# Performance work log

Hardware: AMD Instinct MI355X
Metric: run time of the kernel (lower is better)

## Reference

```python
import jax, jax.numpy as jnp
import numpy as np

B, S, D = 2, 2048, 2048
HQ, HKV, HD, HDV = 32, 8, 64, 64
QPK = HQ // HKV
EPS = 1e-5


def setup_inputs() -> dict:
    key = jax.random.key(0)
    ks = jax.random.split(key, 10)
    s = lambda fan_in: 1.0 / np.sqrt(fan_in)
    return {
        'x': jax.random.normal(ks[0], (B, S, D), dtype=jnp.float32),
        'ln_g': jnp.ones((D,), jnp.float32),
        'ln_b': jnp.zeros((D,), jnp.float32),
        'Wq': jax.random.uniform(ks[1], (D, HQ * HD), jnp.float32, -s(D), s(D)),
        'bq': jax.random.uniform(ks[2], (HQ * HD,), jnp.float32, -s(D), s(D)),
        'Wk': jax.random.uniform(ks[3], (D, HKV * HD), jnp.float32, -s(D), s(D)),
        'bk': jax.random.uniform(ks[4], (HKV * HD,), jnp.float32, -s(D), s(D)),
        'Wv': jax.random.uniform(ks[5], (D, HKV * HDV), jnp.float32, -s(D), s(D)),
        'bv': jax.random.uniform(ks[6], (HKV * HDV,), jnp.float32, -s(D), s(D)),
        'Wo': jax.random.uniform(ks[7], (HQ * HDV, D), jnp.float32, -s(HQ * HDV), s(HQ * HDV)),
        'bo': jax.random.uniform(ks[8], (D,), jnp.float32, -s(HQ * HDV), s(HQ * HDV)),
    }


def reference(x, ln_g, ln_b, Wq, bq, Wk, bk, Wv, bv, Wo, bo):
    # LayerNorm
    mu = jnp.mean(x, axis=-1, keepdims=True)
    var = jnp.mean(jnp.square(x - mu), axis=-1, keepdims=True)
    xn = (x - mu) * jax.lax.rsqrt(var + EPS) * ln_g + ln_b

    q = (xn @ Wq + bq).reshape(B, S, HKV, QPK, HD) * (1.0 / np.sqrt(HD))
    k = (xn @ Wk + bk).reshape(B, S, HKV, HD)
    v = (xn @ Wv + bv).reshape(B, S, HKV, HDV)

    # scores: (b, t=query, T=key, h, q_per_kv)
    scores = jnp.einsum('bthqd,bThd->btThq', q, k)
    # causal mask: -inf where T > t (upper triangle above diagonal)
    mask = jnp.triu(jnp.full((S, S), -jnp.inf, dtype=scores.dtype), 1)
    scores = scores + mask[None, :, :, None, None]
    # NOTE: source softmaxes over dim=-4, i.e. the QUERY axis t -> axis=1 here
    scores = jax.nn.softmax(scores, axis=1)
    out = jnp.einsum('btThq,bThd->bthqd', scores, v)
    out = out.reshape(B, S, HQ * HDV)
    return out @ Wo + bo
```

## Files before the change

kernel.cpp:

```cpp
#include <hip/hip_runtime.h>

#define Bb  2
#define Ss  2048
#define Dd  2048
#define HKV 8
#define QPK 4
#define HD  64
#define MR  (Bb * Ss)
#define NQ  2048
#define NKV 512

#define LOG2E 1.4426950408889634f

typedef unsigned short u16;
typedef unsigned int u32;
typedef __attribute__((ext_vector_type(8))) short s16x8;
typedef __attribute__((ext_vector_type(4))) float f32x4;

__device__ __forceinline__ u16 f2bf(float f) {
  unsigned u = __float_as_uint(f);
  u += 0x7fffu + ((u >> 16) & 1u);
  return (u16)(u >> 16);
}

__device__ __forceinline__ void gload16(const u16* g, u16* l) {
  __builtin_amdgcn_global_load_lds(
      (const __attribute__((address_space(1))) unsigned int*)g,
      (__attribute__((address_space(3))) unsigned int*)l, 16, 0, 0);
}

__device__ __forceinline__ u32 cvtpk_bf16(float a, float b) {
  u32 r;
  asm volatile("v_cvt_pk_bf16_f32 %0, %1, %2" : "=v"(r) : "v"(a), "v"(b));
  return r;
}

#define BAR()    asm volatile("s_barrier" ::: "memory")
#define WAITV4() asm volatile("s_waitcnt vmcnt(4)" ::: "memory")
#define WAITV2() asm volatile("s_waitcnt vmcnt(2)" ::: "memory")
#define WAITV0() asm volatile("s_waitcnt vmcnt(0)" ::: "memory")

__global__ __launch_bounds__(256) void ln_kernel(
    const float* __restrict__ x, const float* __restrict__ g,
    const float* __restrict__ be, u16* __restrict__ xn)
{
  int row = blockIdx.x;
  int tid = threadIdx.x;
  const float4* xr = (const float4*)(x + (size_t)row * Dd);
  float4 a = xr[tid];
  float4 b4 = xr[tid + 256];
  float s  = a.x + a.y + a.z + a.w + b4.x + b4.y + b4.z + b4.w;
  float ss = a.x*a.x + a.y*a.y + a.z*a.z + a.w*a.w
           + b4.x*b4.x + b4.y*b4.y + b4.z*b4.z + b4.w*b4.w;
  #pragma unroll
  for (int off = 32; off > 0; off >>= 1) {
    s  += __shfl_down(s, off);
    ss += __shfl_down(ss, off);
  }
  __shared__ float red[8];
  int lane = tid & 63, w = tid >> 6;
  if (lane == 0) { red[w] = s; red[4 + w] = ss; }
  __syncthreads();
  s  = red[0] + red[1] + red[2] + red[3];
  ss = red[4] + red[5] + red[6] + red[7];
  float mu = s * (1.0f / Dd);
  float rs = rsqrtf(ss * (1.0f / Dd) - mu * mu + 1e-5f);

  u16* xo = xn + (size_t)row * Dd;
  const float4* gv4 = (const float4*)g;
  const float4* bv4 = (const float4*)be;
  #pragma unroll
  for (int p = 0; p < 2; ++p) {
    int idx = tid + p * 256;
    float4 xv = (p == 0) ? a : b4;
    float4 gg = gv4[idx], bb = bv4[idx];
    ushort4 pk;
    pk.x = f2bf((xv.x - mu) * rs * gg.x + bb.x);
    pk.y = f2bf((xv.y - mu) * rs * gg.y + bb.y);
    pk.z = f2bf((xv.z - mu) * rs * gg.z + bb.z);
    pk.w = f2bf((xv.w - mu) * rs * gg.w + bb.w);
    *(ushort4*)(xo + idx * 4) = pk;
  }
}

__global__ __launch_bounds__(256) void transpose_all(
    const float* __restrict__ Wq, const float* __restrict__ Wk,
    const float* __restrict__ Wv, const float* __restrict__ Wo,
    u16* __restrict__ wqkvT, u16* __restrict__ woT)
{
  int id = blockIdx.x;
  const float* W; u16* WT; int N, loc;
  if (id < 4096)      { W = Wq; WT = wqkvT;                          N = NQ;  loc = id; }
  else if (id < 5120) { W = Wk; WT = wqkvT + (size_t)NQ * Dd;        N = NKV; loc = id - 4096; }
  else if (id < 6144) { W = Wv; WT = wqkvT + (size_t)(NQ + NKV) * Dd; N = NKV; loc = id - 5120; }
  else                { W = Wo; WT = woT;                            N = NQ;  loc = id - 6144; }
  int nx = N >> 5;
  int n0 = (loc % nx) * 32, k0 = (loc / nx) * 32;

  __shared__ float tile[32][33];
  int tx = threadIdx.x & 31, ty = threadIdx.x >> 5;
  #pragma unroll
  for (int i = 0; i < 4; ++i)
    tile[ty + 8 * i][tx] = W[(size_t)(k0 + ty + 8 * i) * N + n0 + tx];
  __syncthreads();
  #pragma unroll
  for (int i = 0; i < 4; ++i)
    WT[(size_t)(n0 + ty + 8 * i) * Dd + k0 + tx] = f2bf(tile[tx][ty + 8 * i]);
}

__device__ __forceinline__ void gemm8_core(
    const u16* __restrict__ A, const u16* __restrict__ BT, int K,
    int brow, int bcol, u16* __restrict__ As, u16* __restrict__ Bs,
    f32x4 (&acc)[8][4])
{
  const int tid  = threadIdx.x;
  const int lane = tid & 63;
  const int wave = tid >> 6;
  const int wr = wave >> 2, wc = wave & 3;
  const int m16 = lane & 15, quad = lane >> 4;
  const int NT = K >> 6;

  const int r0 = tid >> 3;
  const int sg = (tid & 7) ^ (r0 & 7);
  const u16* Asrc = A  + (size_t)(brow + r0) * K + sg * 8;
  const u16* Bsrc = BT + (size_t)(bcol + r0) * K + sg * 8;
  u16* AsW = As + wave * 512;
  u16* BsW = Bs + wave * 512;
  const size_t a64 = (size_t)64 * K;

  const int sl0 = (quad ^ (m16 & 7)) * 8;
  const int sl1 = ((quad | 4) ^ (m16 & 7)) * 8;
  const u16* Afr = As + wr * 8192 + m16 * 64;
  const u16* Bfr = Bs + (wc >> 1) * 8192 + ((wc & 1) * 64 + m16) * 64;

  #pragma unroll
  for (int h = 0; h < 2; ++h) {
    gload16(Asrc + (size_t)(h * 128) * K, AsW + h * 8192);
    gload16(Asrc + (size_t)(h * 128) * K + a64, AsW + h * 8192 + 4096);
    gload16(Bsrc + (size_t)(h * 128) * K, BsW + h * 8192);
    gload16(Bsrc + (size_t)(h * 128) * K + a64, BsW + h * 8192 + 4096);
  }
  #pragma unroll
  for (int h = 0; h < 2; ++h) {
    gload16(Bsrc + (size_t)(h * 128) * K + 64, BsW + 16384 + h * 8192);
    gload16(Bsrc + (size_t)(h * 128) * K + a64 + 64, BsW + 16384 + h * 8192 + 4096);
  }
  WAITV4();
  BAR();

  for (int t = 0; t < NT; ++t) {
    const int bi = t & 1;
    const u16* Abuf = Afr + bi * 16384;
    const u16* Bbuf = Bfr + bi * 16384;
    s16x8 bfr[4][2];
    #pragma unroll
    for (int ph = 0; ph < 4; ++ph) {
      s16x8 a0k0 = *(const s16x8*)(Abuf + (ph * 2 + 0) * 1024 + sl0);
      s16x8 a0k1 = *(const s16x8*)(Abuf + (ph * 2 + 0) * 1024 + sl1);
      s16x8 a1k0 = *(const s16x8*)(Abuf + (ph * 2 + 1) * 1024 + sl0);
      s16x8 a1k1 = *(const s16x8*)(Abuf + (ph * 2 + 1) * 1024 + sl1);
      if (ph == 0) {
        #pragma unroll
        for (int nj = 0; nj < 4; ++nj) {
          bfr[nj][0] = *(const s16x8*)(Bbuf + nj * 1024 + sl0);
          bfr[nj][1] = *(const s16x8*)(Bbuf + nj * 1024 + sl1);
        }
      }
      if (ph < 2) {
        if (t + 1 < NT) {
          const u16* g = Asrc + (size_t)(ph * 128) * K + (t + 1) * 64;
          u16* l = AsW + (bi ^ 1) * 16384 + ph * 8192;
          gload16(g, l);
          gload16(g + a64, l + 4096);
        }
      } else {
        if (t + 2 < NT) {
          const u16* g = Bsrc + (size_t)((ph - 2) * 128) * K + (t + 2) * 64;
          u16* l = BsW + bi * 16384 + (ph - 2) * 8192;
          gload16(g, l);
          gload16(g + a64, l + 4096);
        }
      }
      BAR();
      __builtin_amdgcn_s_setprio(1);
      #pragma unroll
      for (int nj = 0; nj < 4; ++nj) {
        acc[ph*2+0][nj] = __builtin_amdgcn_mfma_f32_16x16x32_bf16(a0k0, bfr[nj][0], acc[ph*2+0][nj], 0, 0, 0);
        acc[ph*2+0][nj] = __builtin_amdgcn_mfma_f32_16x16x32_bf16(a0k1, bfr[nj][1], acc[ph*2+0][nj], 0, 0, 0);
        acc[ph*2+1][nj] = __builtin_amdgcn_mfma_f32_16x16x32_bf16(a1k0, bfr[nj][0], acc[ph*2+1][nj], 0, 0, 0);
        acc[ph*2+1][nj] = __builtin_amdgcn_mfma_f32_16x16x32_bf16(a1k1, bfr[nj][1], acc[ph*2+1][nj], 0, 0, 0);
      }
      __builtin_amdgcn_s_setprio(0);
      if (ph == 3) {
        if (t + 2 < NT) WAITV4(); else WAITV0();
      }
      BAR();
    }
  }
}

__global__ __launch_bounds__(512) void gemm8_qkv(
    const u16* __restrict__ A, const u16* __restrict__ BT,
    const float* __restrict__ bq, const float* __restrict__ bk,
    const float* __restrict__ bv,
    u16* __restrict__ qb, u16* __restrict__ kb, u16* __restrict__ vT)
{
  __shared__ u16 As[32768];
  __shared__ u16 Bs[32768];
  int nbx = 12;
  int id  = blockIdx.y * nbx + blockIdx.x;
  int nwg = 192;
  int swz = (id & 7) * (nwg >> 3) + (id >> 3);
  int bx = swz % nbx, by = swz / nbx;

  f32x4 acc[8][4] = {};
  gemm8_core(A, BT, Dd, by * 256, bx * 256, As, Bs, acc);

  int lane = threadIdx.x & 63, wave = threadIdx.x >> 6;
  int wr = wave >> 2, wc = wave & 3;
  int m16 = lane & 15, quad = lane >> 4;
  int wcol = (wc >> 1) * 128 + (wc & 1) * 64;

  if (bx < 8) {
    int colb = bx * 256 + wcol;
    #pragma unroll
    for (int nj = 0; nj < 4; ++nj) {
      int col = colb + nj * 16 + m16;
      float bc = bq[col];
      #pragma unroll
      for (int mi = 0; mi < 8; ++mi)
        #pragma unroll
        for (int rr = 0; rr < 4; ++rr) {
          int row = by * 256 + wr * 128 + mi * 16 + quad * 4 + rr;
          qb[(size_t)row * NQ + col] = f2bf((acc[mi][nj][rr] + bc) * (0.125f * LOG2E));
        }
    }
  } else if (bx < 10) {
    int colb = (bx - 8) * 256 + wcol;
    #pragma unroll
    for (int nj = 0; nj < 4; ++nj) {
      int col = colb + nj * 16 + m16;
      float bc = bk[col];
      #pragma unroll
      for (int mi = 0; mi < 8; ++mi)
        #pragma unroll
        for (int rr = 0; rr < 4; ++rr) {
          int row = by * 256 + wr * 128 + mi * 16 + quad * 4 + rr;
          kb[(size_t)row * NKV + col] = f2bf(acc[mi][nj][rr] + bc);
        }
    }
  } else {
    int colb = (bx - 10) * 256 + wcol;
    #pragma unroll
    for (int nj = 0; nj < 4; ++nj) {
      int col = colb + nj * 16 + m16;
      float bc = bv[col];
      #pragma unroll
      for (int mi = 0; mi < 8; ++mi) {
        int row = by * 256 + wr * 128 + mi * 16 + quad * 4;
        int b = row >> 11, t = row & 2047;
        ushort4 pk;
        pk.x = f2bf(acc[mi][nj][0] + bc);
        pk.y = f2bf(acc[mi][nj][1] + bc);
        pk.z = f2bf(acc[mi][nj][2] + bc);
        pk.w = f2bf(acc[mi][nj][3] + bc);
        *(ushort4*)(vT + ((size_t)(b * NKV + col)) * Ss + t) = pk;
      }
    }
  }
}

__global__ __launch_bounds__(512) void gemm8_wo(
    const u16* __restrict__ A, const u16* __restrict__ BT,
    const float* __restrict__ bias, float* __restrict__ C, int N, int K)
{
  __shared__ u16 As[32768];
  __shared__ u16 Bs[16384];
  int nbx = N >> 7;
  int id  = blockIdx.y * nbx + blockIdx.x;
  int nwg = gridDim.x * gridDim.y;
  int swz = (id & 7) * (nwg >> 3) + (id >> 3);
  int bx = swz % nbx, by = swz / nbx;

  const int tid  = threadIdx.x;
  const int lane = tid & 63;
  const int wave = tid >> 6;
  const int wr = wave >> 2, wc = wave & 3;
  const int m16 = lane & 15, quad = lane >> 4;
  const int NT = K >> 6;

  const int r0 = tid >> 3;
  const int sg = (tid & 7) ^ (r0 & 7);
  const u16* Asrc = A  + (size_t)(by * 256 + r0) * K + sg * 8;
  const u16* Bsrc = BT + (size_t)(bx * 128 + r0) * K + sg * 8;
  u16* AsW = As + wave * 512;
  u16* BsW = Bs + wave * 512;
  const size_t a64 = (size_t)64 * K;

  const int sl0 = (quad ^ (m16 & 7)) * 8;
  const int sl1 = ((quad | 4) ^ (m16 & 7)) * 8;
  const u16* Afr = As + wr * 8192 + m16 * 64;
  const u16* Bfr = Bs + (wc * 32 + m16) * 64;

  f32x4 acc[8][2] = {};

  #pragma unroll
  for (int h = 0; h < 2; ++h) {
    gload16(Asrc + (size_t)(h * 128) * K, AsW + h * 8192);
    gload16(Asrc + (size_t)(h * 128) * K + a64, AsW + h * 8192 + 4096);
  }
  gload16(Bsrc, BsW);
  gload16(Bsrc + a64, BsW + 4096);
  gload16(Bsrc + 64, BsW + 8192);
  gload16(Bsrc + a64 + 64, BsW + 8192 + 4096);
  WAITV2();
  BAR();

  for (int t = 0; t < NT; ++t) {
    const int bi = t & 1;
    const u16* Abuf = Afr + bi * 16384;
    const u16* Bbuf = Bfr + bi * 8192;
    s16x8 bfr[2][2];
    #pragma unroll
    for (int ph = 0; ph < 4; ++ph) {
      s16x8 a0k0 = *(const s16x8*)(Abuf + (ph * 2 + 0) * 1024 + sl0);
      s16x8 a0k1 = *(const s16x8*)(Abuf + (ph * 2 + 0) * 1024 + sl1);
      s16x8 a1k0 = *(const s16x8*)(Abuf + (ph * 2 + 1) * 1024 + sl0);
      s16x8 a1k1 = *(const s16x8*)(Abuf + (ph * 2 + 1) * 1024 + sl1);
      if (ph == 0) {
        #pragma unroll
        for (int nj = 0; nj < 2; ++nj) {
          bfr[nj][0] = *(const s16x8*)(Bbuf + nj * 1024 + sl0);
          bfr[nj][1] = *(const s16x8*)(Bbuf + nj * 1024 + sl1);
        }
      }
      if (ph < 2) {
        if (t + 1 < NT) {
          const u16* g = Asrc + (size_t)(ph * 128) * K + (t + 1) * 64;
          u16* l = AsW + (bi ^ 1) * 16384 + ph * 8192;
          gload16(g, l);
          gload16(g + a64, l + 4096);
        }
      } else if (ph == 2) {
        if (t + 2 < NT) {
          const u16* g = Bsrc + (size_t)(t + 2) * 64;
          u16* l = BsW + bi * 8192;
          gload16(g, l);
          gload16(g + a64, l + 4096);
        }
      }
      BAR();
      __builtin_amdgcn_s_setprio(1);
      #pragma unroll
      for (int nj = 0; nj < 2; ++nj) {
        acc[ph*2+0][nj] = __builtin_amdgcn_mfma_f32_16x16x32_bf16(a0k0, bfr[nj][0], acc[ph*2+0][nj], 0, 0, 0);
        acc[ph*2+0][nj] = __builtin_amdgcn_mfma_f32_16x16x32_bf16(a0k1, bfr[nj][1], acc[ph*2+0][nj], 0, 0, 0);
        acc[ph*2+1][nj] = __builtin_amdgcn_mfma_f32_16x16x32_bf16(a1k0, bfr[nj][0], acc[ph*2+1][nj], 0, 0, 0);
        acc[ph*2+1][nj] = __builtin_amdgcn_mfma_f32_16x16x32_bf16(a1k1, bfr[nj][1], acc[ph*2+1][nj], 0, 0, 0);
      }
      __builtin_amdgcn_s_setprio(0);
      if (ph == 3) {
        if (t + 2 < NT) WAITV2(); else WAITV0();
      }
      BAR();
    }
  }

  int colb = bx * 128 + wc * 32;
  #pragma unroll
  for (int nj = 0; nj < 2; ++nj) {
    int col = colb + nj * 16 + m16;
    float bc = bias[col];
    #pragma unroll
    for (int mi = 0; mi < 8; ++mi)
      #pragma unroll
      for (int rr = 0; rr < 4; ++rr) {
        int row = by * 256 + wr * 128 + mi * 16 + quad * 4 + rr;
        C[(size_t)row * N + col] = acc[mi][nj][rr] + bc;
      }
  }
}

__global__ __launch_bounds__(256) void pass_a_mfma(
    const u16* __restrict__ qb, const u16* __restrict__ kb,
    float* __restrict__ cst)
{
  __shared__ u16 Qs[2][64 * 64];
  int combo = blockIdx.x;
  int qk = combo & 3, bh = combo >> 2;
  int b = bh >> 3, h = bh & 7;
  int g = blockIdx.y;
  int tid = threadIdx.x;
  int lane = tid & 63, wave = tid >> 6;
  int m16 = lane & 15, quad = lane >> 4;
  int T0w = g * 128 + wave * 32;

  const u16* kbase = kb + (size_t)b * Ss * NKV + h * HD;
  const u16* qbase = qb + (size_t)b * Ss * NQ + (h * QPK + qk) * HD;

  s16x8 kf[2][2];
  #pragma unroll
  for (int jg = 0; jg < 2; ++jg)
    #pragma unroll
    for (int dc = 0; dc < 2; ++dc)
      kf[jg][dc] = *(const s16x8*)(kbase + (size_t)(T0w + jg * 16 + m16) * NKV + dc * 32 + quad * 8);

  float ms[2] = {-1e30f, -1e30f};
  float ls[2] = {0.f, 0.f};
  int srow  = (wave << 3) + (lane >> 3);
  int slot0 = (lane & 7) ^ (lane >> 3);
  int sl0 = quad ^ (m16 & 7);
  int sl1 = (quad | 4) ^ (m16 & 7);
  int tDiag = T0w & ~63;

  {
    u16* QsW = &Qs[0][(wave * 8) * 64];
    int t0 = g * 128;
    gload16(qbase + (size_t)(t0 + srow) * NQ + slot0 * 8, QsW);
    gload16(qbase + (size_t)(t0 + srow + 32) * NQ + slot0 * 8, QsW + 32 * 64);
  }

  for (int t0 = g * 128; t0 < Ss; t0 += 64) {
    int cur = (t0 >> 6) & 1;
    bool nxt = (t0 + 64 < Ss);
    if (nxt) {
      u16* QsW = &Qs[cur ^ 1][(wave * 8) * 64];
      gload16(qbase + (size_t)(t0 + 64 + srow) * NQ + slot0 * 8, QsW);
      gload16(qbase + (size_t)(t0 + 64 + srow + 32) * NQ + slot0 * 8, QsW + 32 * 64);
      WAITV2();
    } else {
      WAITV0();
    }
    BAR();
    if (t0 + 63 < T0w) { BAR(); continue; }

    const u16* Qc = &Qs[cur][0];
    s16x8 af[4][2];
    #pragma unroll
    for (int i = 0; i < 4; ++i) {
      af[i][0] = *(const s16x8*)(Qc + (i * 16 + m16) * 64 + sl0 * 8);
      af[i][1] = *(const s16x8*)(Qc + (i * 16 + m16) * 64 + sl1 * 8);
    }
    f32x4 acc[4][2];
    #pragma unroll
    for (int i = 0; i < 4; ++i)
      #pragma unroll
      for (int jg = 0; jg < 2; ++jg) {
        f32x4 z = {};
        z = __builtin_amdgcn_mfma_f32_16x16x32_bf16(af[i][0], kf[jg][0], z, 0, 0, 0);
        acc[i][jg] = __builtin_amdgcn_mfma_f32_16x16x32_bf16(af[i][1], kf[jg][1], z, 0, 0, 0);
      }
    if (t0 == tDiag) {
      #pragma unroll
      for (int i = 0; i < 4; ++i)
        #pragma unroll
        for (int jg = 0; jg < 2; ++jg) {
          int tg = t0 + i * 16 + quad * 4;
          int Tg = T0w + jg * 16 + m16;
          #pragma unroll
          for (int r = 0; r < 4; ++r)
            if (tg + r < Tg) acc[i][jg][r] = -3e38f;
        }
    }
    #pragma unroll
    for (int jg = 0; jg < 2; ++jg) {
      float bm = -3e38f;
      #pragma unroll
      for (int i = 0; i < 4; ++i)
        #pragma unroll
        for (int r = 0; r < 4; ++r) bm = fmaxf(bm, acc[i][jg][r]);
      float mn = fmaxf(ms[jg], bm);
      float se = 0.f;
      #pragma unroll
      for (int i = 0; i < 4; ++i)
        #pragma unroll
        for (int r = 0; r < 4; ++r) se += exp2f(acc[i][jg][r] - mn);
      ls[jg] = ls[jg] * exp2f(ms[jg] - mn) + se;
      ms[jg] = mn;
    }
    BAR();
  }
  #pragma unroll
  for (int jg = 0; jg < 2; ++jg) {
    float m = ms[jg], l = ls[jg];
    #pragma unroll
    for (int off = 16; off <= 32; off <<= 1) {
      float mo = __shfl_xor(m, off);
      float lo = __shfl_xor(l, off);
      float mn = fmaxf(m, mo);
      l = l * exp2f(m - mn) + lo * exp2f(mo - mn);
      m = mn;
    }
    if (quad == 0)
      cst[(size_t)(bh * QPK + qk) * Ss + T0w + jg * 16 + m16] = -(m + __log2f(l));
  }
}

__global__ __launch_bounds__(256) void pass_b_mfma(
    const u16* __restrict__ qb, const u16* __restrict__ kb,
    const u16* __restrict__ vT, const float* __restrict__ cst,
    u16* __restrict__ attn)
{
  __shared__ u16 Ks[2][64 * 64];
  __shared__ u16 Vs[2][64 * 64];
  int combo = blockIdx.x;
  int qk = combo & 3, bh = combo >> 2;
  int b = bh >> 3, h = bh & 7;
  int g = 31 - blockIdx.y;
  int tid = threadIdx.x;
  int lane = tid & 63, wave = tid >> 6;
  int m16 = lane & 15, quad = lane >> 4;
  int trow = g * 64 + wave * 16;

  const u16* qbase = qb + (size_t)b * Ss * NQ + (h * QPK + qk) * HD;
  const u16* kbase = kb + (size_t)b * Ss * NKV + h * HD;
  const u16* vbase = vT + (size_t)(bh * 64) * Ss;
  const float* cbase = cst + (size_t)(bh * QPK + qk) * Ss;

  s16x8 qf[2];
  #pragma unroll
  for (int dc = 0; dc < 2; ++dc)
    qf[dc] = *(const s16x8*)(qbase + (size_t)(trow + m16) * NQ + dc * 32 + quad * 8);

  f32x4 oacc[4] = {};
  int srow  = (wave << 3) + (lane >> 3);
  int slot0 = (lane & 7) ^ (lane >> 3);
  int sl0 = quad ^ (m16 & 7);
  int sl1 = (quad | 4) ^ (m16 & 7);
  int Tend = g * 64;

  {
    u16* KsW = &Ks[0][(wave * 8) * 64];
    u16* VsW = &Vs[0][(wave * 8) * 64];
    gload16(kbase + (size_t)srow * NKV + slot0 * 8, KsW);
    gload16(kbase + (size_t)(srow + 32) * NKV + slot0 * 8, KsW + 32 * 64);
    gload16(vbase + (size_t)srow * Ss + slot0 * 8, VsW);
    gload16(vbase + (size_t)(srow + 32) * Ss + slot0 * 8, VsW + 32 * 64);
  }

  for (int T0 = 0; T0 <= Tend; T0 += 64) {
    int cur = (T0 >> 6) & 1;
    bool nxt = (T0 + 64 <= Tend);
    float4 cc[4];
    #pragma unroll
    for (int i = 0; i < 4; ++i)
      cc[i] = *(const float4*)(cbase + T0 + i * 16 + quad * 4);
    __builtin_amdgcn_sched_barrier(0);
    if (nxt) {
      u16* KsW = &Ks[cur ^ 1][(wave * 8) * 64];
      u16* VsW = &Vs[cur ^ 1][(wave * 8) * 64];
      gload16(kbase + (size_t)(T0 + 64 + srow) * NKV + slot0 * 8, KsW);
      gload16(kbase + (size_t)(T0 + 64 + srow + 32) * NKV + slot0 * 8, KsW + 32 * 64);
      gload16(vbase + (size_t)srow * Ss + T0 + 64 + slot0 * 8, VsW);
      gload16(vbase + (size_t)(srow + 32) * Ss + T0 + 64 + slot0 * 8, VsW + 32 * 64);
      WAITV4();
    } else {
      WAITV0();
    }
    BAR();
    bool diag = (T0 == Tend);
    const u16* Kc = &Ks[cur][0];
    const u16* Vc = &Vs[cur][0];
    #pragma unroll
    for (int tc = 0; tc < 2; ++tc) {
      u32 A[2], Bw[2];
      #pragma unroll
      for (int ii = 0; ii < 2; ++ii) {
        int i = tc * 2 + ii;
        s16x8 k0 = *(const s16x8*)(Kc + (i * 16 + m16) * 64 + sl0 * 8);
        s16x8 k1 = *(const s16x8*)(Kc + (i * 16 + m16) * 64 + sl1 * 8);
        float4 c4 = cc[i];
        f32x4 z = {c4.x, c4.y, c4.z, c4.w};
        z = __builtin_amdgcn_mfma_f32_16x16x32_bf16(k0, qf[0], z, 0, 0, 0);
        z = __builtin_amdgcn_mfma_f32_16x16x32_bf16(k1, qf[1], z, 0, 0, 0);
        float w0 = exp2f(z[0]);
        float w1 = exp2f(z[1]);
        float w2 = exp2f(z[2]);
        float w3 = exp2f(z[3]);
        if (diag) {
          int t  = trow + m16;
          int Tg = T0 + i * 16 + quad * 4;
          if (Tg + 0 > t) w0 = 0.f;
          if (Tg + 1 > t) w1 = 0.f;
          if (Tg + 2 > t) w2 = 0.f;
          if (Tg + 3 > t) w3 = 0.f;
        }
        A[ii]  = cvtpk_bf16(w0, w1);
        Bw[ii] = cvtpk_bf16(w2, w3);
      }
      asm volatile("v_permlane32_swap_b32 %0, %1" : "+v"(A[0]),  "+v"(A[1]));
      asm volatile("v_permlane16_swap_b32 %0, %1" : "+v"(A[0]),  "+v"(A[1]));
      asm volatile("v_permlane32_swap_b32 %0, %1" : "+v"(Bw[0]), "+v"(Bw[1]));
      asm volatile("v_permlane16_swap_b32 %0, %1" : "+v"(Bw[0]), "+v"(Bw[1]));
      union { uint4 u; s16x8 v; } pu;
      pu.u.x = A[0]; pu.u.y = Bw[0]; pu.u.z = A[1]; pu.u.w = Bw[1];
      s16x8 pa = pu.v;
      #pragma unroll
      for (int dj = 0; dj < 4; ++dj) {
        int vsl = (quad | (tc << 2)) ^ (m16 & 7);
        s16x8 vf = *(const s16x8*)(Vc + (dj * 16 + m16) * 64 + vsl * 8);
        oacc[dj] = __builtin_amdgcn_mfma_f32_16x16x32_bf16(pa, vf, oacc[dj], 0, 0, 0);
      }
    }
    BAR();
  }
  u16* abase = attn + (size_t)b * Ss * NQ + (h * QPK + qk) * HD;
  #pragma unroll
  for (int dj = 0; dj < 4; ++dj)
    #pragma unroll
    for (int r = 0; r < 4; ++r)
      abase[(size_t)(trow + quad * 4 + r) * NQ + dj * 16 + m16] = f2bf(oacc[dj][r]);
}

extern "C" void kernel_launch(void* const* d_in, const int* in_sizes, int n_in,
                              void* d_out, int out_size, void* d_ws, size_t ws_size,
                              hipStream_t stream)
{
  (void)in_sizes; (void)n_in; (void)out_size; (void)ws_size;
  const float* x   = (const float*)d_in[0];
  const float* lng = (const float*)d_in[1];
  const float* lnb = (const float*)d_in[2];
  const float* Wq  = (const float*)d_in[3];
  const float* bq  = (const float*)d_in[4];
  const float* Wk  = (const float*)d_in[5];
  const float* bk  = (const float*)d_in[6];
  const float* Wv  = (const float*)d_in[7];
  const float* bv  = (const float*)d_in[8];
  const float* Wo  = (const float*)d_in[9];
  const float* bo  = (const float*)d_in[10];
  float* out = (float*)d_out;

  char* ws = (char*)d_ws;
  size_t off = 0;
  auto take = [&](size_t bytes) -> char* {
    char* p = ws + off;
    off += (bytes + 255) & ~(size_t)255;
    return p;
  };
  u16*    xnb   = (u16*)take((size_t)MR * Dd * 2);
  u16*    wqkvT = (u16*)take((size_t)(NQ + 2 * NKV) * Dd * 2);
  u16*    woT   = (u16*)take((size_t)Dd * NQ * 2);
  u16*    qbB   = (u16*)take((size_t)MR * NQ * 2);
  u16*    kbB   = (u16*)take((size_t)MR * NKV * 2);
  u16*    vTb   = (u16*)take((size_t)MR * NKV * 2);
  float*  cst   = (float*)take((size_t)Bb * HKV * QPK * Ss * 4);
  u16*    attnb = (u16*)take((size_t)MR * NQ * 2);

  ln_kernel<<<MR, 256, 0, stream>>>(x, lng, lnb, xnb);
  transpose_all<<<10240, 256, 0, stream>>>(Wq, Wk, Wv, Wo, wqkvT, woT);

  gemm8_qkv<<<dim3(12, 16), 512, 0, stream>>>(xnb, wqkvT, bq, bk, bv, qbB, kbB, vTb);

  pass_a_mfma<<<dim3(64, 16), 256, 0, stream>>>(qbB, kbB, cst);
  pass_b_mfma<<<dim3(64, 32), 256, 0, stream>>>(qbB, kbB, vTb, cst, attnb);

  gemm8_wo<<<dim3(16, 16), 512, 0, stream>>>(attnb, woT, bo, out, Dd, NQ);
}
```

Before: 382.0 us.

## Prefetch A two tiles ahead and hoist all LDS fragment reads per k-tile

Both GEMM kernels now prefetch A tiles two k-steps ahead, matching B, instead of one step ahead. All A and B fragments for a k-tile are read from LDS at the top of the iteration into registers. An lgkmcnt(0) wait after phase 0 lets the prefetch safely overwrite the same buffer in later phases. The aim is deeper latency hiding for global-to-LDS loads and fewer LDS read stalls between MFMA groups. The cost is higher register pressure, which may reduce occupancy or cause spills.

```diff
diff --git a/kernel.cpp b/kernel.cpp
--- a/kernel.cpp
+++ b/kernel.cpp
@@ -36,9 +36,12 @@
 }
 
 #define BAR()    asm volatile("s_barrier" ::: "memory")
+#define WAITV8() asm volatile("s_waitcnt vmcnt(8)" ::: "memory")
+#define WAITV6() asm volatile("s_waitcnt vmcnt(6)" ::: "memory")
 #define WAITV4() asm volatile("s_waitcnt vmcnt(4)" ::: "memory")
 #define WAITV2() asm volatile("s_waitcnt vmcnt(2)" ::: "memory")
 #define WAITV0() asm volatile("s_waitcnt vmcnt(0)" ::: "memory")
+#define LGKM0()  asm volatile("s_waitcnt lgkmcnt(0)" ::: "memory")
 
 __global__ __launch_bounds__(256) void ln_kernel(
     const float* __restrict__ x, const float* __restrict__ g,
@@ -126,7 +129,8 @@
   const u16* Bsrc = BT + (size_t)(bcol + r0) * K + sg * 8;
   u16* AsW = As + wave * 512;
   u16* BsW = Bs + wave * 512;
-  const size_t a64 = (size_t)64 * K;
+  const size_t a64  = (size_t)64 * K;
+  const size_t a128 = (size_t)128 * K;
 
   const int sl0 = (quad ^ (m16 & 7)) * 8;
   const int sl1 = ((quad | 4) ^ (m16 & 7)) * 8;
@@ -134,65 +138,68 @@
   const u16* Bfr = Bs + (wc >> 1) * 8192 + ((wc & 1) * 64 + m16) * 64;
 
   #pragma unroll
-  for (int h = 0; h < 2; ++h) {
-    gload16(Asrc + (size_t)(h * 128) * K, AsW + h * 8192);
-    gload16(Asrc + (size_t)(h * 128) * K + a64, AsW + h * 8192 + 4096);
-    gload16(Bsrc + (size_t)(h * 128) * K, BsW + h * 8192);
-    gload16(Bsrc + (size_t)(h * 128) * K + a64, BsW + h * 8192 + 4096);
-  }
-  #pragma unroll
-  for (int h = 0; h < 2; ++h) {
-    gload16(Bsrc + (size_t)(h * 128) * K + 64, BsW + 16384 + h * 8192);
-    gload16(Bsrc + (size_t)(h * 128) * K + a64 + 64, BsW + 16384 + h * 8192 + 4096);
-  }
-  WAITV4();
+  for (int tt = 0; tt < 2; ++tt) {
+    #pragma unroll
+    for (int h = 0; h < 2; ++h) {
+      gload16(Asrc + h * a128 + tt * 64,       AsW + tt * 16384 + h * 8192);
+      gload16(Asrc + h * a128 + a64 + tt * 64, AsW + tt * 16384 + h * 8192 + 4096);
+      gload16(Bsrc + h * a128 + tt * 64,       BsW + tt * 16384 + h * 8192);
+      gload16(Bsrc + h * a128 + a64 + tt * 64, BsW + tt * 16384 + h * 8192 + 4096);
+    }
+  }
+  WAITV8();
   BAR();
 
   for (int t = 0; t < NT; ++t) {
     const int bi = t & 1;
     const u16* Abuf = Afr + bi * 16384;
     const u16* Bbuf = Bfr + bi * 16384;
-    s16x8 bfr[4][2];
+    const bool st = (t + 2 < NT);
+    const u16* Ag2 = Asrc + (size_t)(t + 2) * 64;
+    const u16* Bg2 = Bsrc + (size_t)(t + 2) * 64;
+    u16* AsN = AsW + bi * 16384;
+    u16* BsN = BsW + bi * 16384;
+
+    s16x8 af[8][2], bfr[4][2];
+    #pragma unroll
+    for (int mi = 0; mi < 8; ++mi) {
+      af[mi][0] = *(const s16x8*)(Abuf + mi * 1024 + sl0);
+      af[mi][1] = *(const s16x8*)(Abuf + mi * 1024 + sl1);
+    }
+    #pragma unroll
+    for (int nj = 0; nj < 4; ++nj) {
+      bfr[nj][0] = *(const s16x8*)(Bbuf + nj * 1024 + sl0);
+      bfr[nj][1] = *(const s16x8*)(Bbuf + nj * 1024 + sl1);
+    }
     #pragma unroll
     for (int ph = 0; ph < 4; ++ph) {
-      s16x8 a0k0 = *(const s16x8*)(Abuf + (ph * 2 + 0) * 1024 + sl0);
-      s16x8 a0k1 = *(const s16x8*)(Abuf + (ph * 2 + 0) * 1024 + sl1);
-      s16x8 a1k0 = *(const s16x8*)(Abuf + (ph * 2 + 1) * 1024 + sl0);
-      s16x8 a1k1 = *(const s16x8*)(Abuf + (ph * 2 + 1) * 1024 + sl1);
-      if (ph == 0) {
-        #pragma unroll
-        for (int nj = 0; nj < 4; ++nj) {
-          bfr[nj][0] = *(const s16x8*)(Bbuf + nj * 1024 + sl0);
-          bfr[nj][1] = *(const s16x8*)(Bbuf + nj * 1024 + sl1);
-        }
-      }
-      if (ph < 2) {
-        if (t + 1 < NT) {
-          const u16* g = Asrc + (size_t)(ph * 128) * K + (t + 1) * 64;
-          u16* l = AsW + (bi ^ 1) * 16384 + ph * 8192;
-          gload16(g, l);
-          gload16(g + a64, l + 4096);
-        }
-      } else {
-        if (t + 2 < NT) {
-          const u16* g = Bsrc + (size_t)((ph - 2) * 128) * K + (t + 2) * 64;
-          u16* l = BsW + bi * 16384 + (ph - 2) * 8192;
-          gload16(g, l);
-          gload16(g + a64, l + 4096);
+      if (st) {
+        if (ph == 1) {
+          gload16(Ag2,       AsN);
+          gload16(Ag2 + a64, AsN + 4096);
+        } else if (ph == 2) {
+          gload16(Ag2 + a128,       AsN + 8192);
+          gload16(Ag2 + a128 + a64, AsN + 8192 + 4096);
+          gload16(Bg2,       BsN);
+          gload16(Bg2 + a64, BsN + 4096);
+        } else if (ph == 3) {
+          gload16(Bg2 + a128,       BsN + 8192);
+          gload16(Bg2 + a128 + a64, BsN + 8192 + 4096);
         }
       }
       BAR();
       __builtin_amdgcn_s_setprio(1);
       #pragma unroll
       for (int nj = 0; nj < 4; ++nj) {
-        acc[ph*2+0][nj] = __builtin_amdgcn_mfma_f32_16x16x32_bf16(a0k0, bfr[nj][0], acc[ph*2+0][nj], 0, 0, 0);
-        acc[ph*2+0][nj] = __builtin_amdgcn_mfma_f32_16x16x32_bf16(a0k1, bfr[nj][1], acc[ph*2+0][nj], 0, 0, 0);
-        acc[ph*2+1][nj] = __builtin_amdgcn_mfma_f32_16x16x32_bf16(a1k0, bfr[nj][0], acc[ph*2+1][nj], 0, 0, 0);
-        acc[ph*2+1][nj] = __builtin_amdgcn_mfma_f32_16x16x32_bf16(a1k1, bfr[nj][1], acc[ph*2+1][nj], 0, 0, 0);
+        acc[ph*2+0][nj] = __builtin_amdgcn_mfma_f32_16x16x32_bf16(af[ph*2+0][0], bfr[nj][0], acc[ph*2+0][nj], 0, 0, 0);
+        acc[ph*2+0][nj] = __builtin_amdgcn_mfma_f32_16x16x32_bf16(af[ph*2+0][1], bfr[nj][1], acc[ph*2+0][nj], 0, 0, 0);
+        acc[ph*2+1][nj] = __builtin_amdgcn_mfma_f32_16x16x32_bf16(af[ph*2+1][0], bfr[nj][0], acc[ph*2+1][nj], 0, 0, 0);
+        acc[ph*2+1][nj] = __builtin_amdgcn_mfma_f32_16x16x32_bf16(af[ph*2+1][1], bfr[nj][1], acc[ph*2+1][nj], 0, 0, 0);
       }
       __builtin_amdgcn_s_setprio(0);
+      if (ph == 0) LGKM0();
       if (ph == 3) {
-        if (t + 2 < NT) WAITV4(); else WAITV0();
+        if (st) WAITV8(); else WAITV0();
       }
       BAR();
     }
@@ -295,7 +302,8 @@
   const u16* Bsrc = BT + (size_t)(bx * 128 + r0) * K + sg * 8;
   u16* AsW = As + wave * 512;
   u16* BsW = Bs + wave * 512;
-  const size_t a64 = (size_t)64 * K;
+  const size_t a64  = (size_t)64 * K;
+  const size_t a128 = (size_t)128 * K;
 
   const int sl0 = (quad ^ (m16 & 7)) * 8;
   const int sl1 = ((quad | 4) ^ (m16 & 7)) * 8;
@@ -305,62 +313,66 @@
   f32x4 acc[8][2] = {};
 
   #pragma unroll
-  for (int h = 0; h < 2; ++h) {
-    gload16(Asrc + (size_t)(h * 128) * K, AsW + h * 8192);
-    gload16(Asrc + (size_t)(h * 128) * K + a64, AsW + h * 8192 + 4096);
-  }
-  gload16(Bsrc, BsW);
-  gload16(Bsrc + a64, BsW + 4096);
-  gload16(Bsrc + 64, BsW + 8192);
-  gload16(Bsrc + a64 + 64, BsW + 8192 + 4096);
-  WAITV2();
+  for (int tt = 0; tt < 2; ++tt) {
+    #pragma unroll
+    for (int h = 0; h < 2; ++h) {
+      gload16(Asrc + h * a128 + tt * 64,       AsW + tt * 16384 + h * 8192);
+      gload16(Asrc + h * a128 + a64 + tt * 64, AsW + tt * 16384 + h * 8192 + 4096);
+    }
+    gload16(Bsrc + tt * 64,       BsW + tt * 8192);
+    gload16(Bsrc + a64 + tt * 64, BsW + tt * 8192 + 4096);
+  }
+  WAITV6();
   BAR();
 
   for (int t = 0; t < NT; ++t) {
     const int bi = t & 1;
     const u16* Abuf = Afr + bi * 16384;
     const u16* Bbuf = Bfr + bi * 8192;
-    s16x8 bfr[2][2];
+    const bool st = (t + 2 < NT);
+    const u16* Ag2 = Asrc + (size_t)(t + 2) * 64;
+    const u16* Bg2 = Bsrc + (size_t)(t + 2) * 64;
+    u16* AsN = AsW + bi * 16384;
+    u16* BsN = BsW + bi * 8192;
+
+    s16x8 af[8][2], bfr[2][2];
+    #pragma unroll
+    for (int mi = 0; mi < 8; ++mi) {
+      af[mi][0] = *(const s16x8*)(Abuf + mi * 1024 + sl0);
+      af[mi][1] = *(const s16x8*)(Abuf + mi * 1024 + sl1);
+    }
+    #pragma unroll
+    for (int nj = 0; nj < 2; ++nj) {
+      bfr[nj][0] = *(const s16x8*)(Bbuf + nj * 1024 + sl0);
+      bfr[nj][1] = *(const s16x8*)(Bbuf + nj * 1024 + sl1);
+    }
     #pragma unroll
     for (int ph = 0; ph < 4; ++ph) {
-      s16x8 a0k0 = *(const s16x8*)(Abuf + (ph * 2 + 0) * 1024 + sl0);
-      s16x8 a0k1 = *(const s16x8*)(Abuf + (ph * 2 + 0) * 1024 + sl1);
-      s16x8 a1k0 = *(const s16x8*)(Abuf + (ph * 2 + 1) * 1024 + sl0);
-      s16x8 a1k1 = *(const s16x8*)(Abuf + (ph * 2 + 1) * 1024 + sl1);
-      if (ph == 0) {
-        #pragma unroll
-        for (int nj = 0; nj < 2; ++nj) {
-          bfr[nj][0] = *(const s16x8*)(Bbuf + nj * 1024 + sl0);
-          bfr[nj][1] = *(const s16x8*)(Bbuf + nj * 1024 + sl1);
-        }
-      }
-      if (ph < 2) {
-        if (t + 1 < NT) {
-          const u16* g = Asrc + (size_t)(ph * 128) * K + (t + 1) * 64;
-          u16* l = AsW + (bi ^ 1) * 16384 + ph * 8192;
-          gload16(g, l);
-          gload16(g + a64, l + 4096);
-        }
-      } else if (ph == 2) {
-        if (t + 2 < NT) {
-          const u16* g = Bsrc + (size_t)(t + 2) * 64;
-          u16* l = BsW + bi * 8192;
-          gload16(g, l);
-          gload16(g + a64, l + 4096);
+      if (st) {
+        if (ph == 1) {
+          gload16(Ag2,       AsN);
+          gload16(Ag2 + a64, AsN + 4096);
+        } else if (ph == 2) {
+          gload16(Ag2 + a128,       AsN + 8192);
+          gload16(Ag2 + a128 + a64, AsN + 8192 + 4096);
+        } else if (ph == 3) {
+          gload16(Bg2,       BsN);
+          gload16(Bg2 + a64, BsN + 4096);
         }
       }
       BAR();
       __builtin_amdgcn_s_setprio(1);
       #pragma unroll
       for (int nj = 0; nj < 2; ++nj) {
-        acc[ph*2+0][nj] = __builtin_amdgcn_mfma_f32_16x16x32_bf16(a0k0, bfr[nj][0], acc[ph*2+0][nj], 0, 0, 0);
-        acc[ph*2+0][nj] = __builtin_amdgcn_mfma_f32_16x16x32_bf16(a0k1, bfr[nj][1], acc[ph*2+0][nj], 0, 0, 0);
-        acc[ph*2+1][nj] = __builtin_amdgcn_mfma_f32_16x16x32_bf16(a1k0, bfr[nj][0], acc[ph*2+1][nj], 0, 0, 0);
-        acc[ph*2+1][nj] = __builtin_amdgcn_mfma_f32_16x16x32_bf16(a1k1, bfr[nj][1], acc[ph*2+1][nj], 0, 0, 0);
+        acc[ph*2+0][nj] = __builtin_amdgcn_mfma_f32_16x16x32_bf16(af[ph*2+0][0], bfr[nj][0], acc[ph*2+0][nj], 0, 0, 0);
+        acc[ph*2+0][nj] = __builtin_amdgcn_mfma_f32_16x16x32_bf16(af[ph*2+0][1], bfr[nj][1], acc[ph*2+0][nj], 0, 0, 0);
+        acc[ph*2+1][nj] = __builtin_amdgcn_mfma_f32_16x16x32_bf16(af[ph*2+1][0], bfr[nj][0], acc[ph*2+1][nj], 0, 0, 0);
+        acc[ph*2+1][nj] = __builtin_amdgcn_mfma_f32_16x16x32_bf16(af[ph*2+1][1], bfr[nj][1], acc[ph*2+1][nj], 0, 0, 0);
       }
       __builtin_amdgcn_s_setprio(0);
+      if (ph == 0) LGKM0();
       if (ph == 3) {
-        if (t + 2 < NT) WAITV2(); else WAITV0();
+        if (st) WAITV6(); else WAITV0();
       }
       BAR();
     }
```

Measured after the change: 364.3 us. -4.6%, faster.
